# Performance work log

Measured on AMD Instinct MI355X. Metric: run time of the kernel, lower is better.

## Reference

```python
import jax, jax.numpy as jnp
import numpy as np

DIM = 1024
HEADS = 8
EV = DIM  # dim*expand - dim with expand=2
P = 2.0   # power-softmax exponent
EPS = 1e-5


def setup_inputs() -> dict:
    key = jax.random.key(0)
    k1, k2, k3 = jax.random.split(key, 3)
    B, L = 4, 2048
    x = jax.random.normal(k1, (B, L, DIM), dtype=jnp.float32)
    gamma = jnp.ones((DIM,), dtype=jnp.float32)
    beta = jnp.zeros((DIM,), dtype=jnp.float32)
    # torch nn.Linear weights are [out_features, in_features]
    w_qkv = jax.random.normal(k2, (5 * DIM, DIM), dtype=jnp.float32) * (DIM ** -0.5)
    w_out = jax.random.normal(k3, (DIM, 2 * DIM), dtype=jnp.float32) * ((2 * DIM) ** -0.5)
    return {"x": x, "gamma": gamma, "beta": beta, "w_qkv": w_qkv, "w_out": w_out}


def _layernorm(x, gamma, beta):
    xf = x.astype(jnp.float32)
    mu = jnp.mean(xf, axis=-1, keepdims=True)
    var = jnp.mean(jnp.square(xf - mu), axis=-1, keepdims=True)
    return ((xf - mu) * jax.lax.rsqrt(var + EPS)) * gamma + beta


def _p_softmax(scores, scale, p):
    # scores: [B,H,L,L] with -inf on masked entries
    s = scores.astype(jnp.float32) * scale
    if p == 1.0:
        return jax.nn.softmax(s, axis=-1)
    lse = jax.nn.logsumexp(s * p, axis=-1, keepdims=True) / p
    return jnp.exp(s - lse)


def _attention(q, k, v, heads, p):
    B, L, D = q.shape
    hd = D // heads
    q = q.reshape(B, L, heads, hd).transpose(0, 2, 1, 3)  # bhld
    k = k.reshape(B, L, heads, hd).transpose(0, 2, 1, 3)
    v = v.reshape(B, L, heads, hd).transpose(0, 2, 1, 3)
    scores = jnp.einsum('bhqd,bhkd->bhqk', q, k)
    mask = jnp.tril(jnp.ones((L, L), dtype=bool))
    scores = jnp.where(mask, scores, -jnp.inf)
    probs = _p_softmax(scores, hd ** -0.5, p).astype(q.dtype)
    out = jnp.einsum('bhqk,bhkd->bhqd', probs, v)
    return out.transpose(0, 2, 1, 3).reshape(B, L, D)


def reference(x, gamma, beta, w_qkv, w_out):
    h = _layernorm(x, gamma, beta).astype(x.dtype)
    proj = h @ w_qkv.T  # [B,L,5*DIM]
    q, k, v, lin, pre = jnp.split(proj, np.cumsum([DIM, DIM, DIM, EV]), axis=-1)
    attn = _attention(q, k, v, HEADS, P)
    branch = jnp.concatenate([lin * jax.nn.gelu(pre, approximate=False), attn], axis=-1)
    return x + branch @ w_out.T
```

## Files before the change

kernel.cpp:

```cpp
#include <hip/hip_runtime.h>
#include <hip/hip_bf16.h>
#include <math.h>

#define DIMD 1024
#define LSEQ 2048
#define BATCH 4
#define NHEAD 8
#define HD 128
#define NROWS (BATCH*LSEQ)
#define PROJC (5*DIMD)
#define BRC (2*DIMD)

typedef __attribute__((ext_vector_type(8))) short short8;
typedef __attribute__((ext_vector_type(4))) short short4v;
typedef __attribute__((ext_vector_type(4))) float floatx4;

__device__ __forceinline__ float bf2f(short s) {
  unsigned int u = ((unsigned int)(unsigned short)s) << 16;
  return __builtin_bit_cast(float, u);
}
__device__ __forceinline__ short f2bf(float f) {
  unsigned int u = __builtin_bit_cast(unsigned int, f);
  unsigned int lsb = (u >> 16) & 1u;
  u += 0x7fffu + lsb;
  return (short)(u >> 16);
}

__device__ __forceinline__ void gl2lds16(const short* g, short* l) {
  __builtin_amdgcn_global_load_lds(
      (const __attribute__((address_space(1))) unsigned int*)(unsigned long long)g,
      (__attribute__((address_space(3))) unsigned int*)(unsigned int)(unsigned long long)l,
      16, 0, 0);
}

__device__ __forceinline__ void wgbar() {
  asm volatile("" ::: "memory");
  __builtin_amdgcn_s_barrier();
  asm volatile("" ::: "memory");
}

__global__ __launch_bounds__(256) void cvt2_kernel(const float* __restrict__ s1,
    short* __restrict__ d1, int n1_4, const float* __restrict__ s2,
    short* __restrict__ d2, int n2_4) {
  int i = blockIdx.x * 256 + threadIdx.x;
  const float* src; short* dst;
  if (i < n1_4) { src = s1; dst = d1; }
  else { i -= n1_4; if (i >= n2_4) return; src = s2; dst = d2; }
  float4 v = *(const float4*)(src + (size_t)i * 4);
  short4v o;
  o[0] = f2bf(v.x); o[1] = f2bf(v.y); o[2] = f2bf(v.z); o[3] = f2bf(v.w);
  *(short4v*)(dst + (size_t)i * 4) = o;
}

__global__ __launch_bounds__(256) void ln_kernel(const float* __restrict__ x,
    const float* __restrict__ gamma, const float* __restrict__ beta,
    short* __restrict__ h) {
  int row = blockIdx.x;
  int c = threadIdx.x * 4;
  const float* xr = x + (size_t)row * DIMD;
  float4 v = *(const float4*)(xr + c);
  float f[4] = {v.x, v.y, v.z, v.w};
  float sum = 0.f, sq = 0.f;
  for (int i = 0; i < 4; ++i) { sum += f[i]; sq += f[i]*f[i]; }
  for (int off = 1; off < 64; off <<= 1) {
    sum += __shfl_xor(sum, off);
    sq  += __shfl_xor(sq, off);
  }
  __shared__ float red[8];
  int wid = threadIdx.x >> 6;
  if ((threadIdx.x & 63) == 0) { red[wid*2] = sum; red[wid*2+1] = sq; }
  __syncthreads();
  sum = red[0]+red[2]+red[4]+red[6];
  sq  = red[1]+red[3]+red[5]+red[7];
  float mu = sum * (1.0f/DIMD);
  float var = sq * (1.0f/DIMD) - mu*mu;
  float rstd = rsqrtf(var + 1e-5f);
  float4 g = *(const float4*)(gamma + c);
  float4 bb = *(const float4*)(beta + c);
  float gg[4] = {g.x, g.y, g.z, g.w};
  float bv[4] = {bb.x, bb.y, bb.z, bb.w};
  short4v o;
  for (int i = 0; i < 4; ++i)
    o[i] = f2bf((f[i] - mu) * rstd * gg[i] + bv[i]);
  *(short4v*)(h + (size_t)row * DIMD + c) = o;
}

__device__ __forceinline__ void rd_a(const short* base, int s0, int s1,
                                     short8 (&a)[4][2]) {
#pragma unroll
  for (int m = 0; m < 4; ++m) {
    a[m][0] = *(const short8*)(base + m*16*64 + s0);
    a[m][1] = *(const short8*)(base + m*16*64 + s1);
  }
}
__device__ __forceinline__ void rd_b(const short* base, int s0, int s1,
                                     short8 (&b)[2][2]) {
#pragma unroll
  for (int n = 0; n < 2; ++n) {
    b[n][0] = *(const short8*)(base + n*16*64 + s0);
    b[n][1] = *(const short8*)(base + n*16*64 + s1);
  }
}
template<int QM, int QN>
__device__ __forceinline__ void qmm(const short8 (&a)[4][2], const short8 (&b)[2][2],
                                    floatx4 (&acc)[8][4]) {
  __builtin_amdgcn_s_setprio(1);
#pragma unroll
  for (int m = 0; m < 4; ++m)
#pragma unroll
    for (int n = 0; n < 2; ++n) {
      floatx4 c = acc[QM*4+m][QN*2+n];
      c = __builtin_amdgcn_mfma_f32_16x16x32_bf16(a[m][0], b[n][0], c, 0, 0, 0);
      c = __builtin_amdgcn_mfma_f32_16x16x32_bf16(a[m][1], b[n][1], c, 0, 0, 0);
      acc[QM*4+m][QN*2+n] = c;
    }
  __builtin_amdgcn_s_setprio(0);
}
template<int QN>
__device__ __forceinline__ void qmm2(const short8 (&a)[4][2], const short8 (&b)[2][2],
                                     floatx4 (&acc)[4][4]) {
  __builtin_amdgcn_s_setprio(1);
#pragma unroll
  for (int m = 0; m < 4; ++m)
#pragma unroll
    for (int n = 0; n < 2; ++n) {
      floatx4 c = acc[m][QN*2+n];
      c = __builtin_amdgcn_mfma_f32_16x16x32_bf16(a[m][0], b[n][0], c, 0, 0, 0);
      c = __builtin_amdgcn_mfma_f32_16x16x32_bf16(a[m][1], b[n][1], c, 0, 0, 0);
      acc[m][QN*2+n] = c;
    }
  __builtin_amdgcn_s_setprio(0);
}
__device__ __forceinline__ void stg2(const short* p, int K, short* lds) {
  gl2lds16(p, lds);
  gl2lds16(p + (size_t)64*K, lds + 64*64);
}
__device__ __forceinline__ void stg4(const short* p, int K, short* lds, int koff) {
  stg2(p + koff, K, lds);
  stg2(p + (size_t)128*K + koff, K, lds + 128*64);
}

__global__ __launch_bounds__(512, 2) void gemm256(const short* __restrict__ A,
    const short* __restrict__ W, short* __restrict__ C, int M, int N, int K) {
  __shared__ __align__(16) short AsF[2*256*64];
  __shared__ __align__(16) short WsF[2*256*64];
  const int tid = threadIdx.x;
  const int lane = tid & 63, wv = tid >> 6;
  const int wm = wv >> 2, wn = wv & 3;
  const int quad = lane >> 4, l16 = lane & 15;

  const int nbx = N >> 8;
  int cpx = gridDim.x >> 3;
  int orig = blockIdx.x;
  int wg = (orig & 7) * cpx + (orig >> 3);
  int bx = wg % nbx, by = wg / nbx;
  const int row0 = by << 8, col0 = bx << 8;

  const int lrow = lane >> 3;
  const int sslot = (lane & 7) ^ lrow;
  const short* pA = A + (size_t)(row0 + wv*8 + lrow) * K + sslot*8;
  const short* pW = W + (size_t)(col0 + wv*8 + lrow) * K + sslot*8;
  short* stA = AsF + wv*8*64;
  short* stW = WsF + wv*8*64;
  const short* aB = AsF + (wm*128 + l16)*64;
  const short* wB = WsF + (wn*64 + l16)*64;
  const int s0 = (quad ^ (l16 & 7)) << 3;
  const int s1 = s0 ^ 32;

  floatx4 acc[8][4] = {};
  short8 a[4][2], b0[2][2], b1[2][2];

  const int nktm = (K >> 6) - 1;

  stg4(pA, K, stA, 0);
  stg4(pW, K, stW, 0);
  stg4(pA, K, stA + 16384, 64);
  asm volatile("s_waitcnt vmcnt(4)" ::: "memory");
  wgbar();

  const int NT = K >> 6;
  for (int t = 0; t < NT; ++t) {
    const int cur = (t & 1) << 14;
    const int nxt = cur ^ 16384;
    const int kw1 = ((t + 1) & nktm) << 6;
    const int ka2 = ((t + 2) & nktm) << 6;
    rd_a(aB + cur, s0, s1, a);
    rd_b(wB + cur, s0, s1, b0);
    stg4(pW, K, stW + nxt, kw1);
    wgbar();
    qmm<0,0>(a, b0, acc);
    rd_b(wB + cur + 32*64, s0, s1, b1);
    wgbar();
    qmm<0,1>(a, b1, acc);
    rd_a(aB + cur + 64*64, s0, s1, a);
    wgbar();
    qmm<1,1>(a, b1, acc);
    wgbar();
    stg4(pA, K, stA + cur, ka2);
    qmm<1,0>(a, b0, acc);
    asm volatile("s_waitcnt vmcnt(4)" ::: "memory");
    wgbar();
  }
  asm volatile("s_waitcnt vmcnt(0)" ::: "memory");

#pragma unroll
  for (int i = 0; i < 8; ++i) {
    int r0 = row0 + wm*128 + i*16 + quad*4;
#pragma unroll
    for (int j = 0; j < 4; ++j) {
      int cc = col0 + wn*64 + j*16 + l16;
#pragma unroll
      for (int r = 0; r < 4; ++r)
        C[(size_t)(r0 + r) * N + cc] = f2bf(acc[i][j][r]);
    }
  }
}

__global__ __launch_bounds__(512, 2) void gemm2(const short* __restrict__ A,
    const short* __restrict__ W, const float* __restrict__ X,
    float* __restrict__ out, int M, int N, int K) {
  __shared__ __align__(16) short As2[2*128*64];
  __shared__ __align__(16) short Ws2[2*256*64];
  const int tid = threadIdx.x;
  const int lane = tid & 63, wv = tid >> 6;
  const int wm = wv >> 2, wn = wv & 3;
  const int quad = lane >> 4, l16 = lane & 15;

  const int nbx = N >> 8;
  int cpx = gridDim.x >> 3;
  int orig = blockIdx.x;
  int wg = (orig & 7) * cpx + (orig >> 3);
  int bx = wg % nbx, by = wg / nbx;
  const int row0 = by << 7, col0 = bx << 8;

  const int lrow = lane >> 3;
  const int sslot = (lane & 7) ^ lrow;
  const short* pA = A + (size_t)(row0 + wv*8 + lrow) * K + sslot*8;
  const short* pW = W + (size_t)(col0 + wv*8 + lrow) * K + sslot*8;
  short* stA = As2 + wv*8*64;
  short* stW = Ws2 + wv*8*64;
  const short* aB = As2 + (wm*64 + l16)*64;
  const short* wB = Ws2 + (wn*64 + l16)*64;
  const int s0 = (quad ^ (l16 & 7)) << 3;
  const int s1 = s0 ^ 32;

  floatx4 acc[4][4] = {};
  short8 a[4][2], b0[2][2], b1[2][2];

  const int nktm = (K >> 6) - 1;

  stg2(pA, K, stA);
  stg4(pW, K, stW, 0);
  stg2(pA + 64, K, stA + 8192);
  asm volatile("s_waitcnt vmcnt(2)" ::: "memory");
  wgbar();

  const int NT = K >> 6;
  for (int t = 0; t < NT; ++t) {
    const int curA = (t & 1) << 13;
    const int curW = (t & 1) << 14;
    const int nxtW = curW ^ 16384;
    const int kw1 = ((t + 1) & nktm) << 6;
    const int ka2 = ((t + 2) & nktm) << 6;
    rd_a(aB + curA, s0, s1, a);
    rd_b(wB + curW, s0, s1, b0);
    stg4(pW, K, stW + nxtW, kw1);
    wgbar();
    qmm2<0>(a, b0, acc);
    rd_b(wB + curW + 32*64, s0, s1, b1);
    wgbar();
    stg2(pA + ka2, K, stA + curA);
    qmm2<1>(a, b1, acc);
    asm volatile("s_waitcnt vmcnt(2)" ::: "memory");
    wgbar();
  }
  asm volatile("s_waitcnt vmcnt(0)" ::: "memory");

#pragma unroll
  for (int i = 0; i < 4; ++i) {
    int r0 = row0 + wm*64 + i*16 + quad*4;
#pragma unroll
    for (int j = 0; j < 4; ++j) {
      int cc = col0 + wn*64 + j*16 + l16;
#pragma unroll
      for (int r = 0; r < 4; ++r) {
        size_t idx = (size_t)(r0 + r) * N + cc;
        out[idx] = acc[i][j][r] + X[idx];
      }
    }
  }
}

__global__ __launch_bounds__(256) void gelu_kernel(const short* __restrict__ proj,
    short* __restrict__ branch) {
  int row = blockIdx.x;
  int c = threadIdx.x * 4;
  const short* pr = proj + (size_t)row * PROJC;
  short4v lin = *(const short4v*)(pr + 3*DIMD + c);
  short4v pre = *(const short4v*)(pr + 4*DIMD + c);
  short4v o;
  for (int i = 0; i < 4; ++i) {
    float xx = bf2f(pre[i]);
    float g = 0.5f * xx * (1.f + erff(xx * 0.70710678118654752f));
    o[i] = f2bf(bf2f(lin[i]) * g);
  }
  *(short4v*)(branch + (size_t)row * BRC + c) = o;
}

__global__ __launch_bounds__(256) void vt_kernel(const short* __restrict__ proj,
    short* __restrict__ vt) {
  int bh = blockIdx.y;
  int b = bh >> 3, hh = bh & 7;
  int l0 = blockIdx.x * 64;
  __shared__ short Ls[64][136];
  int tid = threadIdx.x;
  int r = tid >> 4, c = (tid & 15) * 8;
  const short* Vp = proj + (size_t)b * LSEQ * PROJC + 2*DIMD + hh*HD;
  for (int p = 0; p < 4; ++p)
    *(short8*)&Ls[r + p*16][c] = *(const short8*)(Vp + (size_t)(l0 + r + p*16) * PROJC + c);
  __syncthreads();
  int d = tid >> 1, lh = (tid & 1) * 32;
  short* outp = vt + ((size_t)bh * HD + d) * LSEQ + l0 + lh;
  for (int g = 0; g < 4; ++g) {
    short8 o;
    for (int j = 0; j < 8; ++j) o[j] = Ls[lh + g*8 + j][d];
    *(short8*)(outp + g*8) = o;
  }
}

__global__ __launch_bounds__(512) void attn_kernel(const short* __restrict__ proj,
    const short* __restrict__ vt, short* __restrict__ branch) {
  int bh = blockIdx.y;
  int b = bh >> 3, hh = bh & 7;
  int gx = blockIdx.x;
  int gsel = (bh < 16) ? gx : (15 - gx);
  int tid = threadIdx.x;
  int wv = tid >> 6, lane = tid & 63, quad = lane >> 4, l16 = lane & 15;
  int qsel = 2*gsel + ((wv < 4) ? 0 : 1);
  int qw = qsel * 64 + (wv & 3) * 16;

  const short* Qp  = proj + (size_t)b * LSEQ * PROJC + hh*HD;
  const short* Kp  = Qp + DIMD;
  const short* VTp = vt + (size_t)bh * HD * LSEQ;

  __shared__ short Ks[64][136];
  __shared__ short Vs[128][76];
  __shared__ short Ps[8][16][44];

  short8 qf[4];
  {
    const short* qrow = Qp + (size_t)(qw + l16) * PROJC;
    for (int s = 0; s < 4; ++s) qf[s] = *(const short8*)(qrow + s*32 + quad*8);
  }
  float lsum[4] = {0.f, 0.f, 0.f, 0.f};
  floatx4 O[8] = {};

  const float scale = 0.08838834764831845f;
  int NT = 2*gsel + 2;
  int krow = tid >> 4;
  int kcol = (tid & 15) * 8;
  int vd = tid >> 2;
  int vk = (tid & 3) * 8;

  short8 kv0 = *(const short8*)(Kp + (size_t)(krow) * PROJC + kcol);
  short8 kv1 = *(const short8*)(Kp + (size_t)(32 + krow) * PROJC + kcol);
  short8 vv0 = *(const short8*)(VTp + (size_t)vd * LSEQ + vk);
  short8 vv1 = *(const short8*)(VTp + (size_t)vd * LSEQ + 32 + vk);

  for (int kt = 0; kt < NT; ++kt) {
    int kb64 = kt * 64;
    __syncthreads();
    *(short8*)&Ks[krow][kcol]      = kv0;
    *(short8*)&Ks[krow + 32][kcol] = kv1;
    *(short8*)&Vs[vd][vk]          = vv0;
    *(short8*)&Vs[vd][32 + vk]     = vv1;
    {
      int ktn = (kt + 1 < NT) ? (kt + 1) : kt;
      int kb64n = ktn * 64;
      kv0 = *(const short8*)(Kp + (size_t)(kb64n + krow) * PROJC + kcol);
      kv1 = *(const short8*)(Kp + (size_t)(kb64n + 32 + krow) * PROJC + kcol);
      vv0 = *(const short8*)(VTp + (size_t)vd * LSEQ + kb64n + vk);
      vv1 = *(const short8*)(VTp + (size_t)vd * LSEQ + kb64n + 32 + vk);
    }
    __syncthreads();
    for (int hf = 0; hf < 2; ++hf) {
      int kb = kb64 + hf*32;
      if (kb <= qw + 15) {
        floatx4 s0 = {0.f,0.f,0.f,0.f}, s1 = {0.f,0.f,0.f,0.f};
        for (int s = 0; s < 4; ++s) {
          short8 kf0 = *(const short8*)&Ks[hf*32 + l16][s*32 + quad*8];
          short8 kf1 = *(const short8*)&Ks[hf*32 + 16 + l16][s*32 + quad*8];
          s0 = __builtin_amdgcn_mfma_f32_16x16x32_bf16(qf[s], kf0, s0, 0, 0, 0);
          s1 = __builtin_amdgcn_mfma_f32_16x16x32_bf16(qf[s], kf1, s1, 0, 0, 0);
        }
        int c0 = kb + l16, c1 = kb + 16 + l16;
        for (int r = 0; r < 4; ++r) {
          int q = qw + quad*4 + r;
          float w0 = (c0 <= q) ? __expf(s0[r] * scale) : 0.f;
          float w1 = (c1 <= q) ? __expf(s1[r] * scale) : 0.f;
          lsum[r] += w0*w0 + w1*w1;
          Ps[wv][quad*4+r][l16]      = f2bf(w0);
          Ps[wv][quad*4+r][16 + l16] = f2bf(w1);
        }
        asm volatile("s_waitcnt lgkmcnt(0)" ::: "memory");
        short8 pf = *(const short8*)&Ps[wv][l16][quad*8];
        for (int t8 = 0; t8 < 8; ++t8) {
          short8 vf = *(const short8*)&Vs[t8*16 + l16][hf*32 + quad*8];
          O[t8] = __builtin_amdgcn_mfma_f32_16x16x32_bf16(pf, vf, O[t8], 0, 0, 0);
        }
      }
    }
  }
  for (int r = 0; r < 4; ++r) {
    float l = lsum[r];
    for (int off = 1; off < 16; off <<= 1) l += __shfl_xor(l, off);
    float inv = rsqrtf(l);
    int q = qw + quad*4 + r;
    short* orow = branch + ((size_t)(b*LSEQ + q)) * BRC + DIMD + hh*HD;
    for (int t8 = 0; t8 < 8; ++t8)
      orow[t8*16 + l16] = f2bf(O[t8][r] * inv);
  }
}

extern "C" void kernel_launch(void* const* d_in, const int* in_sizes, int n_in,
                              void* d_out, int out_size, void* d_ws, size_t ws_size,
                              hipStream_t stream) {
  const float* x     = (const float*)d_in[0];
  const float* gamma = (const float*)d_in[1];
  const float* beta  = (const float*)d_in[2];
  const float* w_qkv = (const float*)d_in[3];
  const float* w_out = (const float*)d_in[4];
  float* out = (float*)d_out;

  char* ws = (char*)d_ws;
  short* h      = (short*)ws;
  short* proj   = (short*)(ws + (size_t)16*1024*1024);
  short* branch = (short*)(ws + (size_t)96*1024*1024);
  short* wq     = (short*)(ws + (size_t)128*1024*1024);
  short* wo     = (short*)(ws + (size_t)138*1024*1024);
  short* vt     = h;

  int n1 = PROJC*DIMD/4, n2 = DIMD*BRC/4;
  cvt2_kernel<<<(n1 + n2 + 255)/256, 256, 0, stream>>>(w_qkv, wq, n1, w_out, wo, n2);
  ln_kernel<<<NROWS, 256, 0, stream>>>(x, gamma, beta, h);
  gemm256<<<dim3((NROWS/256)*(PROJC/256)), 512, 0, stream>>>(h, wq, proj,
                                                             NROWS, PROJC, DIMD);
  gelu_kernel<<<NROWS, 256, 0, stream>>>(proj, branch);
  vt_kernel<<<dim3(LSEQ/64, BATCH*NHEAD), 256, 0, stream>>>(proj, vt);
  attn_kernel<<<dim3(16, BATCH*NHEAD), 512, 0, stream>>>(proj, vt, branch);
  gemm2<<<dim3(256), 512, 0, stream>>>(branch, wo, x, out, NROWS, DIMD, BRC);
}
```

Baseline: 322.4 us.

## Fuse V transpose into QKV GEMM epilogue and merge conversion with layernorm

The QKV projection GEMM now writes the V columns directly in transposed per-head layout through an LDS staging patch, removing the separate transpose kernel and its read/write of V. The weight conversion and layernorm kernels are merged into one launch, and attention MFMA sections get raised wave priority. The transposed V buffer now aliases the final output buffer, which gemm2 overwrites later. The extra LDS passes add barriers to the V-column tiles of the GEMM.

```diff
diff --git a/kernel.cpp b/kernel.cpp
--- a/kernel.cpp
+++ b/kernel.cpp
@@ -39,23 +39,25 @@
   asm volatile("" ::: "memory");
 }
 
-__global__ __launch_bounds__(256) void cvt2_kernel(const float* __restrict__ s1,
-    short* __restrict__ d1, int n1_4, const float* __restrict__ s2,
-    short* __restrict__ d2, int n2_4) {
-  int i = blockIdx.x * 256 + threadIdx.x;
-  const float* src; short* dst;
-  if (i < n1_4) { src = s1; dst = d1; }
-  else { i -= n1_4; if (i >= n2_4) return; src = s2; dst = d2; }
-  float4 v = *(const float4*)(src + (size_t)i * 4);
-  short4v o;
-  o[0] = f2bf(v.x); o[1] = f2bf(v.y); o[2] = f2bf(v.z); o[3] = f2bf(v.w);
-  *(short4v*)(dst + (size_t)i * 4) = o;
-}
-
-__global__ __launch_bounds__(256) void ln_kernel(const float* __restrict__ x,
-    const float* __restrict__ gamma, const float* __restrict__ beta,
-    short* __restrict__ h) {
-  int row = blockIdx.x;
+__global__ __launch_bounds__(256) void pre_kernel(
+    const float* __restrict__ x, const float* __restrict__ gamma,
+    const float* __restrict__ beta, short* __restrict__ h,
+    const float* __restrict__ s1, short* __restrict__ d1, int n1_4,
+    const float* __restrict__ s2, short* __restrict__ d2, int n2_4,
+    int nblk_cvt) {
+  int bid = blockIdx.x;
+  if (bid < nblk_cvt) {
+    int i = bid * 256 + threadIdx.x;
+    const float* src; short* dst;
+    if (i < n1_4) { src = s1; dst = d1; }
+    else { i -= n1_4; if (i >= n2_4) return; src = s2; dst = d2; }
+    float4 v = *(const float4*)(src + (size_t)i * 4);
+    short4v o;
+    o[0] = f2bf(v.x); o[1] = f2bf(v.y); o[2] = f2bf(v.z); o[3] = f2bf(v.w);
+    *(short4v*)(dst + (size_t)i * 4) = o;
+    return;
+  }
+  int row = bid - nblk_cvt;
   int c = threadIdx.x * 4;
   const float* xr = x + (size_t)row * DIMD;
   float4 v = *(const float4*)(xr + c);
@@ -141,9 +143,11 @@
 }
 
 __global__ __launch_bounds__(512, 2) void gemm256(const short* __restrict__ A,
-    const short* __restrict__ W, short* __restrict__ C, int M, int N, int K) {
-  __shared__ __align__(16) short AsF[2*256*64];
-  __shared__ __align__(16) short WsF[2*256*64];
+    const short* __restrict__ W, short* __restrict__ C, short* __restrict__ VT,
+    int M, int N, int K) {
+  __shared__ __align__(16) short SH[4*256*64];
+  short* AsF = SH;
+  short* WsF = SH + 2*256*64;
   const int tid = threadIdx.x;
   const int lane = tid & 63, wv = tid >> 6;
   const int wm = wv >> 2, wn = wv & 3;
@@ -203,15 +207,45 @@
   }
   asm volatile("s_waitcnt vmcnt(0)" ::: "memory");
 
-#pragma unroll
-  for (int i = 0; i < 8; ++i) {
-    int r0 = row0 + wm*128 + i*16 + quad*4;
-#pragma unroll
-    for (int j = 0; j < 4; ++j) {
-      int cc = col0 + wn*64 + j*16 + l16;
-#pragma unroll
-      for (int r = 0; r < 4; ++r)
-        C[(size_t)(r0 + r) * N + cc] = f2bf(acc[i][j][r]);
+  const bool isV = (col0 >= 2*DIMD) && (col0 < 3*DIMD);
+  if (!isV) {
+#pragma unroll
+    for (int i = 0; i < 8; ++i) {
+      int r0 = row0 + wm*128 + i*16 + quad*4;
+#pragma unroll
+      for (int j = 0; j < 4; ++j) {
+        int cc = col0 + wn*64 + j*16 + l16;
+#pragma unroll
+        for (int r = 0; r < 4; ++r)
+          C[(size_t)(r0 + r) * N + cc] = f2bf(acc[i][j][r]);
+      }
+    }
+  } else {
+    for (int pass = 0; pass < 2; ++pass) {
+      wgbar();
+      if (wm == pass) {
+        short* patch = SH + wn*8448;
+#pragma unroll
+        for (int j = 0; j < 4; ++j) {
+#pragma unroll
+          for (int i = 0; i < 8; ++i) {
+            short4v p;
+#pragma unroll
+            for (int r = 0; r < 4; ++r) p[r] = f2bf(acc[i][j][r]);
+            *(short4v*)&patch[(j*16 + l16)*132 + i*16 + quad*4] = p;
+          }
+        }
+        asm volatile("s_waitcnt lgkmcnt(0)" ::: "memory");
+        int cv = col0 - 2*DIMD + wn*64 + lane;
+        int hh = cv >> 7, dd = cv & 127;
+        int grow = row0 + wm*128;
+        int bb = grow >> 11, ll = grow & 2047;
+        short* dst = VT + (((size_t)(bb*NHEAD + hh)*HD + dd)*LSEQ + ll);
+        const short* prow = &patch[lane*132];
+#pragma unroll
+        for (int g8 = 0; g8 < 16; ++g8)
+          *(short8*)(dst + g8*8) = *(const short8*)(prow + g8*8);
+      }
     }
   }
 }
@@ -305,27 +339,6 @@
     o[i] = f2bf(bf2f(lin[i]) * g);
   }
   *(short4v*)(branch + (size_t)row * BRC + c) = o;
-}
-
-__global__ __launch_bounds__(256) void vt_kernel(const short* __restrict__ proj,
-    short* __restrict__ vt) {
-  int bh = blockIdx.y;
-  int b = bh >> 3, hh = bh & 7;
-  int l0 = blockIdx.x * 64;
-  __shared__ short Ls[64][136];
-  int tid = threadIdx.x;
-  int r = tid >> 4, c = (tid & 15) * 8;
-  const short* Vp = proj + (size_t)b * LSEQ * PROJC + 2*DIMD + hh*HD;
-  for (int p = 0; p < 4; ++p)
-    *(short8*)&Ls[r + p*16][c] = *(const short8*)(Vp + (size_t)(l0 + r + p*16) * PROJC + c);
-  __syncthreads();
-  int d = tid >> 1, lh = (tid & 1) * 32;
-  short* outp = vt + ((size_t)bh * HD + d) * LSEQ + l0 + lh;
-  for (int g = 0; g < 4; ++g) {
-    short8 o;
-    for (int j = 0; j < 8; ++j) o[j] = Ls[lh + g*8 + j][d];
-    *(short8*)(outp + g*8) = o;
-  }
 }
 
 __global__ __launch_bounds__(512) void attn_kernel(const short* __restrict__ proj,
@@ -387,12 +400,14 @@
       int kb = kb64 + hf*32;
       if (kb <= qw + 15) {
         floatx4 s0 = {0.f,0.f,0.f,0.f}, s1 = {0.f,0.f,0.f,0.f};
+        __builtin_amdgcn_s_setprio(1);
         for (int s = 0; s < 4; ++s) {
           short8 kf0 = *(const short8*)&Ks[hf*32 + l16][s*32 + quad*8];
           short8 kf1 = *(const short8*)&Ks[hf*32 + 16 + l16][s*32 + quad*8];
           s0 = __builtin_amdgcn_mfma_f32_16x16x32_bf16(qf[s], kf0, s0, 0, 0, 0);
           s1 = __builtin_amdgcn_mfma_f32_16x16x32_bf16(qf[s], kf1, s1, 0, 0, 0);
         }
+        __builtin_amdgcn_s_setprio(0);
         int c0 = kb + l16, c1 = kb + 16 + l16;
         for (int r = 0; r < 4; ++r) {
           int q = qw + quad*4 + r;
@@ -404,10 +419,12 @@
         }
         asm volatile("s_waitcnt lgkmcnt(0)" ::: "memory");
         short8 pf = *(const short8*)&Ps[wv][l16][quad*8];
+        __builtin_amdgcn_s_setprio(1);
         for (int t8 = 0; t8 < 8; ++t8) {
           short8 vf = *(const short8*)&Vs[t8*16 + l16][hf*32 + quad*8];
           O[t8] = __builtin_amdgcn_mfma_f32_16x16x32_bf16(pf, vf, O[t8], 0, 0, 0);
         }
+        __builtin_amdgcn_s_setprio(0);
       }
     }
   }
@@ -438,15 +455,16 @@
   short* branch = (short*)(ws + (size_t)96*1024*1024);
   short* wq     = (short*)(ws + (size_t)128*1024*1024);
   short* wo     = (short*)(ws + (size_t)138*1024*1024);
-  short* vt     = h;
+  short* vt     = (short*)out;
 
   int n1 = PROJC*DIMD/4, n2 = DIMD*BRC/4;
-  cvt2_kernel<<<(n1 + n2 + 255)/256, 256, 0, stream>>>(w_qkv, wq, n1, w_out, wo, n2);
-  ln_kernel<<<NROWS, 256, 0, stream>>>(x, gamma, beta, h);
-  gemm256<<<dim3((NROWS/256)*(PROJC/256)), 512, 0, stream>>>(h, wq, proj,
+  int nblk_cvt = (n1 + n2 + 255)/256;
+  pre_kernel<<<nblk_cvt + NROWS, 256, 0, stream>>>(x, gamma, beta, h,
+                                                   w_qkv, wq, n1, w_out, wo, n2,
+                                                   nblk_cvt);
+  gemm256<<<dim3((NROWS/256)*(PROJC/256)), 512, 0, stream>>>(h, wq, proj, vt,
                                                              NROWS, PROJC, DIMD);
   gelu_kernel<<<NROWS, 256, 0, stream>>>(proj, branch);
-  vt_kernel<<<dim3(LSEQ/64, BATCH*NHEAD), 256, 0, stream>>>(proj, vt);
   attn_kernel<<<dim3(16, BATCH*NHEAD), 512, 0, stream>>>(proj, vt, branch);
   gemm2<<<dim3(256), 512, 0, stream>>>(branch, wo, x, out, NROWS, DIMD, BRC);
 }
```

Measured after the change: 312.8 us. 3.0% less time.
